# Kernel tuning notes

Hardware: AMD Instinct MI355X
Metric: run time of the kernel (lower is better)

## Reference

```python
import jax, jax.numpy as jnp
import numpy as np

B, T, D = 16, 4096, 64
K = 4096              # num_embeddings
DECAY = 0.99
COMMITMENT = 0.25
EPS = 1e-5


def setup_inputs() -> dict:
    key = jax.random.key(0)
    k1, k2 = jax.random.split(key)
    inputs = jax.random.normal(k1, (B, T, D), dtype=jnp.float32)
    # torch init: uniform_(-1/K, 1/K); _ema_w initialized to a copy of weight
    weight = jax.random.uniform(k2, (K, D), dtype=jnp.float32, minval=-1.0 / K, maxval=1.0 / K)
    return {
        "inputs": inputs,
        "weight": weight,
        "ema_cluster_size": jnp.zeros((K,), jnp.float32),
        "ema_w": weight,
    }


def reference(inputs, weight, ema_cluster_size, ema_w):
    b, t, d = inputs.shape
    flat = inputs.reshape(-1, d)                                   # [N, D]
    dist = (jnp.sum(flat * flat, axis=1, keepdims=True)
            + jnp.sum(weight * weight, axis=1)
            - 2.0 * flat @ weight.T)
    idx = jnp.argmin(dist, axis=1)                                 # [N]
    quantized = weight[idx].reshape(inputs.shape)                  # gather [B,T,D]

    # --- EMA codebook update (torch.no_grad path; one-hot matmuls == segment sums) ---
    counts = jax.ops.segment_sum(jnp.ones((flat.shape[0],), flat.dtype), idx, num_segments=K)
    cs = ema_cluster_size * DECAY + (1.0 - DECAY) * counts
    n = jnp.sum(cs)
    cs = (cs + EPS) / (n + K * EPS) * n                            # Laplace smoothing
    dw = jax.ops.segment_sum(flat, idx, num_segments=K)            # encodings.T @ flat
    new_ema_w = ema_w * DECAY + (1.0 - DECAY) * dw
    new_weight = new_ema_w / cs[:, None]

    # --- losses (on pre-update codebook, as in torch) ---
    e_latent = jnp.mean((jax.lax.stop_gradient(quantized) - inputs) ** 2)
    q_latent = jnp.mean((quantized - jax.lax.stop_gradient(inputs)) ** 2)
    loss = q_latent + COMMITMENT * e_latent

    # straight-through estimator
    quantized_st = inputs + jax.lax.stop_gradient(quantized - inputs)
    encoding_indices = idx.reshape(b, t)
    return quantized_st, loss, encoding_indices, new_weight, cs, new_ema_w
```

## Files before the change

kernel.cpp:

```cpp
#include <hip/hip_runtime.h>
#include <math.h>

#define NROWS 65536
#define DDIM  64
#define KCODE 4096
#define NSPLIT 2
#define KSPL  (KCODE / NSPLIT)
#define STEPS (KSPL / 16)

#define O_Q    0
#define O_LOSS 4194304
#define O_IDX  4194305
#define O_NW   4259841
#define O_CS   4521985
#define O_NEW  4526081

#define O_A      262144
#define O_B2     327680
#define O_CNT   1000000
#define O_OFF   1010000
#define O_CUR   1020000
#define O_ORD   1030000
#define O_LP    (O_NW + 131074)

typedef _Float16 f16x8 __attribute__((ext_vector_type(8)));
typedef float    f32x4 __attribute__((ext_vector_type(4)));

__global__ __launch_bounds__(256)
void vq_prep(const float* __restrict__ x, const float* __restrict__ w,
             float* __restrict__ out, unsigned long long* __restrict__ keys) {
    int i = blockIdx.x * 256 + threadIdx.x;
    {
        const int k = i >> 6, j = i & 63;
        float E = w[i] * 4096.0f;
        _Float16 h = (_Float16)E;
        float r = E - (float)h;
        _Float16 lo = (_Float16)(r * 4096.0f);
        const size_t pos = (size_t)(k >> 4) * 2048 + (size_t)(j >> 5) * 512
                         + (size_t)((j >> 3) & 3) * 128 + (size_t)(k & 15) * 8
                         + (size_t)(j & 7);
        ((_Float16*)out)[pos] = h;
        ((_Float16*)out)[pos + 1024] = lo;
    }
    if (i < NROWS) keys[i] = 0xFFFFFFFFFFFFFFFFULL;
    if (i < KCODE) ((unsigned*)(out + O_CNT))[i] = 0u;
    if ((i & 3) == 0) {
        const int row = i >> 2;
        const float4* xr = (const float4*)(x + (size_t)row * DDIM);
        float ax = 0.f, ay = 0.f, az = 0.f, aw = 0.f;
        #pragma unroll
        for (int j = 0; j < 16; ++j) {
            float4 v = xr[j];
            ax += v.x * v.x; ay += v.y * v.y; az += v.z * v.z; aw += v.w * v.w;
        }
        out[O_A + row] = (ax + ay) + (az + aw);
    }
    if ((i & 63) == 0) {
        const int k = i >> 6;
        const float4* wr = (const float4*)(w + (size_t)k * DDIM);
        float ax = 0.f, ay = 0.f, az = 0.f, aw = 0.f;
        #pragma unroll
        for (int j = 0; j < 16; ++j) {
            float4 v = wr[j];
            ax += v.x * v.x; ay += v.y * v.y; az += v.z * v.z; aw += v.w * v.w;
        }
        out[O_B2 + k] = (ax + ay) + (az + aw);
    }
}

__device__ inline void split8(float4 a, float4 b, f16x8& hi, f16x8& lo) {
    float vv[8] = {a.x, a.y, a.z, a.w, b.x, b.y, b.z, b.w};
    #pragma unroll
    for (int j = 0; j < 8; ++j) {
        float X = vv[j] * 256.0f;
        _Float16 h = (_Float16)X;
        float r = X - (float)h;
        hi[j] = h;
        lo[j] = (_Float16)(r * 4096.0f);
    }
}

__global__ __launch_bounds__(256, 2)
void vq_argmin_mfma(const float* __restrict__ x,
                    const _Float16* __restrict__ etab,
                    const float* __restrict__ Ag,
                    const float* __restrict__ b2g,
                    unsigned long long* __restrict__ keys) {
    __shared__ __align__(16) float b2sh[KSPL + 128];
    const int tid = threadIdx.x;
    const int k0  = blockIdx.y * KSPL;
    #pragma unroll
    for (int j = 0; j < KSPL / 1024; ++j)
        ((float4*)b2sh)[tid + j * 256] = ((const float4*)(b2g + k0))[tid + j * 256];
    __syncthreads();

    const int l   = tid & 63;
    const int w   = tid >> 6;
    const int g   = l >> 4;
    const int c16 = l & 15;
    const int rowbase = blockIdx.x * 256 + w * 64;

    f16x8 xh[4][2], xl[4][2];
    #pragma unroll
    for (int r = 0; r < 4; ++r) {
        const float* xr = x + (size_t)(rowbase + r * 16 + c16) * DDIM + g * 8;
        float4 a0 = *(const float4*)(xr);
        float4 a1 = *(const float4*)(xr + 4);
        float4 a2 = *(const float4*)(xr + 32);
        float4 a3 = *(const float4*)(xr + 36);
        split8(a0, a1, xh[r][0], xl[r][0]);
        split8(a2, a3, xh[r][1], xl[r][1]);
    }
    float A_reg[4][4];
    #pragma unroll
    for (int r = 0; r < 4; ++r)
        #pragma unroll
        for (int v = 0; v < 4; ++v)
            A_reg[r][v] = Ag[rowbase + r * 16 + 4 * g + v];

    float bestv[4][4]; int bidx[4][4];
    #pragma unroll
    for (int r = 0; r < 4; ++r)
        #pragma unroll
        for (int v = 0; v < 4; ++v) { bestv[r][v] = INFINITY; bidx[r][v] = 0; }

    const _Float16* p[2];
    p[0] = etab + (size_t)(k0 >> 4) * 2048 + (size_t)l * 8;
    p[1] = p[0] + 2048;

    f16x8 bh0[2], bh1[2], bl0[2], bl1[2];
    float b2r[2];
    int b2i[2] = {c16, 16 + c16};
    int cbase = k0 + c16;
    const f32x4 fzero = {0.f, 0.f, 0.f, 0.f};

#define LOADB(sl) do {                                       \
        bh0[sl] = *(const f16x8*)(p[sl]);                    \
        bh1[sl] = *(const f16x8*)(p[sl] + 512);              \
        bl0[sl] = *(const f16x8*)(p[sl] + 1024);             \
        bl1[sl] = *(const f16x8*)(p[sl] + 1536);             \
        b2r[sl] = b2sh[b2i[sl]];                             \
        p[sl] += 4096;                                       \
        b2i[sl] += 32;                                       \
    } while (0)

#define COMP(sl) do {                                                             \
        _Pragma("unroll")                                                         \
        for (int r = 0; r < 4; ++r) {                                             \
            f32x4 acc1, acc2;                                                     \
            acc1 = __builtin_amdgcn_mfma_f32_16x16x32_f16(xh[r][0], bh0[sl], fzero, 0, 0, 0); \
            acc1 = __builtin_amdgcn_mfma_f32_16x16x32_f16(xh[r][1], bh1[sl], acc1,  0, 0, 0); \
            acc2 = __builtin_amdgcn_mfma_f32_16x16x32_f16(xl[r][0], bh0[sl], fzero, 0, 0, 0); \
            acc2 = __builtin_amdgcn_mfma_f32_16x16x32_f16(xl[r][1], bh1[sl], acc2,  0, 0, 0); \
            acc2 = __builtin_amdgcn_mfma_f32_16x16x32_f16(xh[r][0], bl0[sl], acc2,  0, 0, 0); \
            acc2 = __builtin_amdgcn_mfma_f32_16x16x32_f16(xh[r][1], bl1[sl], acc2,  0, 0, 0); \
            _Pragma("unroll")                                                     \
            for (int v = 0; v < 4; ++v) {                                         \
                float dotc = fmaf(acc2[v], 0x1p-12f, acc1[v]);                    \
                float t = A_reg[r][v] + b2r[sl];                                  \
                float sc = fmaf(dotc, -0x1p-19f, t);                              \
                bool lt = sc < bestv[r][v];      \
                bestv[r][v] = lt ? sc : bestv[r][v];                              \
                bidx[r][v]  = lt ? cbase : bidx[r][v];                            \
            }                                                                     \
        }                                                                         \
        cbase += 16;                                                              \
    } while (0)

    LOADB(0);
    LOADB(1);

    #pragma unroll 1
    for (int s = 0; s < STEPS; s += 2) {
        COMP(0);
        LOADB(0);
        COMP(1);
        LOADB(1);
    }
#undef LOADB
#undef COMP

    #pragma unroll
    for (int off2 = 1; off2 < 16; off2 <<= 1) {
        #pragma unroll
        for (int r = 0; r < 4; ++r)
            #pragma unroll
            for (int v = 0; v < 4; ++v) {
                float ob = __shfl_xor(bestv[r][v], off2);
                int   oi = __shfl_xor(bidx[r][v], off2);
                if (ob < bestv[r][v] || (ob == bestv[r][v] && oi < bidx[r][v])) {
                    bestv[r][v] = ob; bidx[r][v] = oi;
                }
            }
    }
    if (c16 == 0) {
        #pragma unroll
        for (int r = 0; r < 4; ++r)
            #pragma unroll
            for (int v = 0; v < 4; ++v) {
                const int row = rowbase + r * 16 + 4 * g + v;
                unsigned long long key =
                    ((unsigned long long)__float_as_uint(bestv[r][v]) << 32) |
                    (unsigned)bidx[r][v];
                atomicMin(&keys[row], key);
            }
    }
}

__global__ __launch_bounds__(1024)
void vq_hist(const unsigned long long* __restrict__ keys,
             unsigned* __restrict__ counts) {
    __shared__ unsigned h[KCODE];
    const int tid = threadIdx.x;
    #pragma unroll
    for (int j = 0; j < 4; ++j) h[tid + j * 1024] = 0u;
    __syncthreads();
    const int row = blockIdx.x * 1024 + tid;
    const unsigned k = (unsigned)(keys[row] & 0xFFFFFFFFu);
    atomicAdd(&h[k], 1u);
    __syncthreads();
    #pragma unroll
    for (int j = 0; j < 4; ++j) {
        unsigned v = h[tid + j * 1024];
        if (v) atomicAdd(&counts[tid + j * 1024], v);
    }
}

__global__ __launch_bounds__(1024)
void vq_scan(const unsigned* __restrict__ counts,
             unsigned* __restrict__ offs, unsigned* __restrict__ cursor) {
    __shared__ unsigned red[1024];
    const int tid = threadIdx.x;
    unsigned c[4], tot = 0;
    #pragma unroll
    for (int j = 0; j < 4; ++j) { c[j] = counts[tid * 4 + j]; tot += c[j]; }
    red[tid] = tot;
    __syncthreads();
    for (int s = 1; s < 1024; s <<= 1) {
        unsigned v = (tid >= s) ? red[tid - s] : 0u;
        __syncthreads();
        red[tid] += v;
        __syncthreads();
    }
    unsigned base = red[tid] - tot;
    #pragma unroll
    for (int j = 0; j < 4; ++j) {
        offs[tid * 4 + j] = base;
        cursor[tid * 4 + j] = base;
        base += c[j];
    }
}

__global__ __launch_bounds__(256)
void vq_scatter(const unsigned long long* __restrict__ keys,
                unsigned* __restrict__ cursor, unsigned* __restrict__ order) {
    const int row = blockIdx.x * 256 + threadIdx.x;
    const unsigned k = (unsigned)(keys[row] & 0xFFFFFFFFu);
    const unsigned slot = atomicAdd(&cursor[k], 1u);
    order[slot] = row;
}

__global__ __launch_bounds__(256)
void vq_dw(const float* __restrict__ x, const float* __restrict__ ema_w,
           const unsigned* __restrict__ counts, const unsigned* __restrict__ offs,
           const unsigned* __restrict__ order, float* __restrict__ out) {
    const int tid = threadIdx.x;
    const int lane = tid & 63;
    const int k = blockIdx.x * 4 + (tid >> 6);
    const unsigned cnt = counts[k];
    const unsigned off = offs[k];
    float acc = 0.f;
    for (unsigned i = 0; i < cnt; ++i) {
        const unsigned row = order[off + i];
        acc += x[(size_t)row * DDIM + lane];
    }
    const float e = ema_w[(size_t)k * DDIM + lane];
    out[O_NEW + (size_t)k * DDIM + lane] = fmaf(0.01f, acc, 0.99f * e);
    if (lane == 0) out[O_CS + k] = (float)cnt;
}

__global__ __launch_bounds__(256)
void vq_gather2(const float* __restrict__ x, const float* __restrict__ w,
                const unsigned long long* __restrict__ keys,
                float* __restrict__ out, float* __restrict__ lpart) {
    const int tid = threadIdx.x;
    const int l16 = tid & 15;
    const int row = blockIdx.x * 16 + (tid >> 4);
    const int k = (int)(unsigned)(keys[row] & 0xFFFFFFFFu);
    if (l16 == 0) out[O_IDX + row] = (float)k;

    const float4 w4 = ((const float4*)(w + (size_t)k * DDIM))[l16];
    const float4 x4 = ((const float4*)(x + (size_t)row * DDIM))[l16];
    float4 o;
    o.x = x4.x + (w4.x - x4.x);
    o.y = x4.y + (w4.y - x4.y);
    o.z = x4.z + (w4.z - x4.z);
    o.w = x4.w + (w4.w - x4.w);
    ((float4*)(out + O_Q + (size_t)row * DDIM))[l16] = o;
    float dx = w4.x - x4.x, dy = w4.y - x4.y, dz = w4.z - x4.z, dw_ = w4.w - x4.w;
    float e = dx * dx + dy * dy + dz * dz + dw_ * dw_;
    #pragma unroll
    for (int off = 32; off > 0; off >>= 1) e += __shfl_down(e, off);
    if ((tid & 63) == 0) lpart[blockIdx.x * 4 + (tid >> 6)] = e;
}

__global__ __launch_bounds__(1024)
void vq_cs(const float* __restrict__ ecs, const float* __restrict__ lpart,
           float* __restrict__ out) {
    __shared__ float red[1024];
    __shared__ double dred[1024];
    const int tid = threadIdx.x;
    double dl = 0.0;
    #pragma unroll
    for (int j = 0; j < 16; ++j) dl += (double)lpart[j * 1024 + tid];
    dred[tid] = dl;
    float cs[4];
    float local = 0.f;
    #pragma unroll
    for (int j = 0; j < 4; ++j) {
        int k = j * 1024 + tid;
        float cnt = out[O_CS + k];
        cs[j] = ecs[k] * 0.99f + 0.01f * cnt;
        local += cs[j];
    }
    red[tid] = local;
    for (int s = 512; s > 0; s >>= 1) {
        __syncthreads();
        if (tid < s) { red[tid] += red[tid + s]; dred[tid] += dred[tid + s]; }
    }
    __syncthreads();
    const float n = red[0];
    const float denom = n + 0.04096f;
    #pragma unroll
    for (int j = 0; j < 4; ++j) {
        int k = j * 1024 + tid;
        out[O_CS + k] = (cs[j] + 1e-5f) / denom * n;
    }
    if (tid == 0) out[O_LOSS] = 1.25f * (float)(dred[0] / 4194304.0);
}

__global__ __launch_bounds__(256)
void vq_final(float* __restrict__ out) {
    int i = blockIdx.x * 256 + threadIdx.x;
    if (i >= KCODE * DDIM) return;
    int k = i >> 6;
    out[O_NW + i] = out[O_NEW + i] / out[O_CS + k];
}

extern "C" void kernel_launch(void* const* d_in, const int* in_sizes, int n_in,
                              void* d_out, int out_size, void* d_ws, size_t ws_size,
                              hipStream_t stream) {
    (void)in_sizes; (void)n_in; (void)out_size; (void)d_ws; (void)ws_size;
    const float* x    = (const float*)d_in[0];
    const float* w    = (const float*)d_in[1];
    const float* ecs  = (const float*)d_in[2];
    const float* emaw = (const float*)d_in[3];
    float* out = (float*)d_out;

    const _Float16* etab = (const _Float16*)out;
    const float*    Ag   = out + O_A;
    unsigned long long* keys = (unsigned long long*)(out + O_NW + 1);
    unsigned* counts = (unsigned*)(out + O_CNT);
    unsigned* offs   = (unsigned*)(out + O_OFF);
    unsigned* cursor = (unsigned*)(out + O_CUR);
    unsigned* order  = (unsigned*)(out + O_ORD);
    float*    lpart  = out + O_LP;

    vq_prep       <<<1024, 256, 0, stream>>>(x, w, out, keys);
    vq_argmin_mfma<<<dim3(256, NSPLIT), 256, 0, stream>>>(x, etab, Ag,
                                                          out + O_B2, keys);
    vq_hist       <<<64, 1024, 0, stream>>>(keys, counts);
    vq_scan       <<<1, 1024, 0, stream>>>(counts, offs, cursor);
    vq_scatter    <<<256, 256, 0, stream>>>(keys, cursor, order);
    vq_dw         <<<1024, 256, 0, stream>>>(x, emaw, counts, offs, order, out);
    vq_gather2    <<<4096, 256, 0, stream>>>(x, w, keys, out, lpart);
    vq_cs         <<<1, 1024, 0, stream>>>(ecs, lpart, out);
    vq_final      <<<1024, 256, 0, stream>>>(out);
}
```

Measured before the change: 179.0 us.

## Software-pipeline MFMA and argmin epilogue, halve rows per warp, split codebook four ways

Restructures the argmin kernel so each warp handles 32 rows instead of 64, the codebook is split into four chunks instead of two, and the grid grows to 512x4 blocks with a higher occupancy hint. The MFMA work for one 16-code tile now overlaps with the compare/select epilogue of the previous tile through double-buffered accumulators. The aim is to hide MFMA latency behind the VALU epilogue and raise occupancy. The cost is that each code tile is loaded for fewer rows, so codebook traffic per row doubles, and there are twice as many atomicMin operations on the keys.

```diff
diff --git a/kernel.cpp b/kernel.cpp
--- a/kernel.cpp
+++ b/kernel.cpp
@@ -4,7 +4,7 @@
 #define NROWS 65536
 #define DDIM  64
 #define KCODE 4096
-#define NSPLIT 2
+#define NSPLIT 4
 #define KSPL  (KCODE / NSPLIT)
 #define STEPS (KSPL / 16)
 
@@ -80,29 +80,27 @@
     }
 }
 
-__global__ __launch_bounds__(256, 2)
+__global__ __launch_bounds__(256, 3)
 void vq_argmin_mfma(const float* __restrict__ x,
                     const _Float16* __restrict__ etab,
                     const float* __restrict__ Ag,
                     const float* __restrict__ b2g,
                     unsigned long long* __restrict__ keys) {
-    __shared__ __align__(16) float b2sh[KSPL + 128];
+    __shared__ __align__(16) float b2sh[KSPL];
     const int tid = threadIdx.x;
     const int k0  = blockIdx.y * KSPL;
-    #pragma unroll
-    for (int j = 0; j < KSPL / 1024; ++j)
-        ((float4*)b2sh)[tid + j * 256] = ((const float4*)(b2g + k0))[tid + j * 256];
+    ((float4*)b2sh)[tid] = ((const float4*)(b2g + k0))[tid];
     __syncthreads();
 
     const int l   = tid & 63;
     const int w   = tid >> 6;
     const int g   = l >> 4;
     const int c16 = l & 15;
-    const int rowbase = blockIdx.x * 256 + w * 64;
-
-    f16x8 xh[4][2], xl[4][2];
-    #pragma unroll
-    for (int r = 0; r < 4; ++r) {
+    const int rowbase = blockIdx.x * 128 + w * 32;
+
+    f16x8 xh[2][2], xl[2][2];
+    #pragma unroll
+    for (int r = 0; r < 2; ++r) {
         const float* xr = x + (size_t)(rowbase + r * 16 + c16) * DDIM + g * 8;
         float4 a0 = *(const float4*)(xr);
         float4 a1 = *(const float4*)(xr + 4);
@@ -111,16 +109,16 @@
         split8(a0, a1, xh[r][0], xl[r][0]);
         split8(a2, a3, xh[r][1], xl[r][1]);
     }
-    float A_reg[4][4];
-    #pragma unroll
-    for (int r = 0; r < 4; ++r)
+    float A_reg[2][4];
+    #pragma unroll
+    for (int r = 0; r < 2; ++r)
         #pragma unroll
         for (int v = 0; v < 4; ++v)
             A_reg[r][v] = Ag[rowbase + r * 16 + 4 * g + v];
 
-    float bestv[4][4]; int bidx[4][4];
-    #pragma unroll
-    for (int r = 0; r < 4; ++r)
+    float bestv[2][4]; int bidx[2][4];
+    #pragma unroll
+    for (int r = 0; r < 2; ++r)
         #pragma unroll
         for (int v = 0; v < 4; ++v) { bestv[r][v] = INFINITY; bidx[r][v] = 0; }
 
@@ -129,9 +127,9 @@
     p[1] = p[0] + 2048;
 
     f16x8 bh0[2], bh1[2], bl0[2], bl1[2];
-    float b2r[2];
-    int b2i[2] = {c16, 16 + c16};
-    int cbase = k0 + c16;
+    f32x4 aA1[2], aA2[2], aB1[2], aB2[2];
+    int cbA = k0 + c16;
+    int cbB = k0 + c16 + 16;
     const f32x4 fzero = {0.f, 0.f, 0.f, 0.f};
 
 #define LOADB(sl) do {                                       \
@@ -139,51 +137,59 @@
         bh1[sl] = *(const f16x8*)(p[sl] + 512);              \
         bl0[sl] = *(const f16x8*)(p[sl] + 1024);             \
         bl1[sl] = *(const f16x8*)(p[sl] + 1536);             \
-        b2r[sl] = b2sh[b2i[sl]];                             \
         p[sl] += 4096;                                       \
-        b2i[sl] += 32;                                       \
     } while (0)
 
-#define COMP(sl) do {                                                             \
+#define MFMAB(a1, a2, sl) do {                                                     \
+        _Pragma("unroll")                                                          \
+        for (int r = 0; r < 2; ++r) {                                              \
+            a1[r] = __builtin_amdgcn_mfma_f32_16x16x32_f16(xh[r][0], bh0[sl], fzero, 0, 0, 0); \
+            a1[r] = __builtin_amdgcn_mfma_f32_16x16x32_f16(xh[r][1], bh1[sl], a1[r], 0, 0, 0); \
+            a2[r] = __builtin_amdgcn_mfma_f32_16x16x32_f16(xl[r][0], bh0[sl], fzero, 0, 0, 0); \
+            a2[r] = __builtin_amdgcn_mfma_f32_16x16x32_f16(xl[r][1], bh1[sl], a2[r], 0, 0, 0); \
+            a2[r] = __builtin_amdgcn_mfma_f32_16x16x32_f16(xh[r][0], bl0[sl], a2[r], 0, 0, 0); \
+            a2[r] = __builtin_amdgcn_mfma_f32_16x16x32_f16(xh[r][1], bl1[sl], a2[r], 0, 0, 0); \
+        }                                                                          \
+    } while (0)
+
+#define EPI(a1, a2, cb) do {                                                      \
+        const float b2v = b2sh[(cb) & (KSPL - 1)];           \
         _Pragma("unroll")                                                         \
-        for (int r = 0; r < 4; ++r) {                                             \
-            f32x4 acc1, acc2;                                                     \
-            acc1 = __builtin_amdgcn_mfma_f32_16x16x32_f16(xh[r][0], bh0[sl], fzero, 0, 0, 0); \
-            acc1 = __builtin_amdgcn_mfma_f32_16x16x32_f16(xh[r][1], bh1[sl], acc1,  0, 0, 0); \
-            acc2 = __builtin_amdgcn_mfma_f32_16x16x32_f16(xl[r][0], bh0[sl], fzero, 0, 0, 0); \
-            acc2 = __builtin_amdgcn_mfma_f32_16x16x32_f16(xl[r][1], bh1[sl], acc2,  0, 0, 0); \
-            acc2 = __builtin_amdgcn_mfma_f32_16x16x32_f16(xh[r][0], bl0[sl], acc2,  0, 0, 0); \
-            acc2 = __builtin_amdgcn_mfma_f32_16x16x32_f16(xh[r][1], bl1[sl], acc2,  0, 0, 0); \
+        for (int r = 0; r < 2; ++r) {                                             \
             _Pragma("unroll")                                                     \
             for (int v = 0; v < 4; ++v) {                                         \
-                float dotc = fmaf(acc2[v], 0x1p-12f, acc1[v]);                    \
-                float t = A_reg[r][v] + b2r[sl];                                  \
+                float dotc = fmaf(a2[r][v], 0x1p-12f, a1[r][v]);                  \
+                float t = A_reg[r][v] + b2v;                                      \
                 float sc = fmaf(dotc, -0x1p-19f, t);                              \
                 bool lt = sc < bestv[r][v];      \
                 bestv[r][v] = lt ? sc : bestv[r][v];                              \
-                bidx[r][v]  = lt ? cbase : bidx[r][v];                            \
+                bidx[r][v]  = lt ? (cb) : bidx[r][v];                             \
             }                                                                     \
         }                                                                         \
-        cbase += 16;                                                              \
+        (cb) += 32;                                                               \
     } while (0)
 
     LOADB(0);
     LOADB(1);
+    MFMAB(aA1, aA2, 0);
 
     #pragma unroll 1
     for (int s = 0; s < STEPS; s += 2) {
-        COMP(0);
         LOADB(0);
-        COMP(1);
+        MFMAB(aB1, aB2, 1);
+        EPI(aA1, aA2, cbA);
         LOADB(1);
+        MFMAB(aA1, aA2, 0);
+        EPI(aB1, aB2, cbB);
     }
 #undef LOADB
-#undef COMP
+#undef MFMAB
+#undef EPI
 
     #pragma unroll
     for (int off2 = 1; off2 < 16; off2 <<= 1) {
         #pragma unroll
-        for (int r = 0; r < 4; ++r)
+        for (int r = 0; r < 2; ++r)
             #pragma unroll
             for (int v = 0; v < 4; ++v) {
                 float ob = __shfl_xor(bestv[r][v], off2);
@@ -195,7 +201,7 @@
     }
     if (c16 == 0) {
         #pragma unroll
-        for (int r = 0; r < 4; ++r)
+        for (int r = 0; r < 2; ++r)
             #pragma unroll
             for (int v = 0; v < 4; ++v) {
                 const int row = rowbase + r * 16 + 4 * g + v;
@@ -367,7 +373,7 @@
     float*    lpart  = out + O_LP;
 
     vq_prep       <<<1024, 256, 0, stream>>>(x, w, out, keys);
-    vq_argmin_mfma<<<dim3(256, NSPLIT), 256, 0, stream>>>(x, etab, Ag,
+    vq_argmin_mfma<<<dim3(512, NSPLIT), 256, 0, stream>>>(x, etab, Ag,
                                                           out + O_B2, keys);
     vq_hist       <<<64, 1024, 0, stream>>>(keys, counts);
     vq_scan       <<<1, 1024, 0, stream>>>(counts, offs, cursor);
```

Result: slower. 196.1 us (+9.6%).
